# Kernel optimization log

Hardware: AMD Instinct MI355X
Metric: run time of the kernel (lower is better)

## Reference

```python
import jax, jax.numpy as jnp
import numpy as np
import math

D_MODEL = 1024
NUM_HEADS = 16
N_GROUP = 4
HEAD_DIM = D_MODEL // NUM_HEADS  # 64
KV_DIM = N_GROUP * HEAD_DIM      # 256
BS, SEQ = 2, 2048


def setup_inputs() -> dict:
    key = jax.random.key(0)
    ks = jax.random.split(key, 7)
    s = 0.02
    return {
        "h": jax.random.normal(ks[0], (BS, SEQ, D_MODEL), dtype=jnp.float32),
        "wq_w": jax.random.normal(ks[1], (D_MODEL, D_MODEL), dtype=jnp.float32) * s,
        "wq_b": jnp.zeros((D_MODEL,), dtype=jnp.float32),
        "wk_w": jax.random.normal(ks[2], (KV_DIM, D_MODEL), dtype=jnp.float32) * s,
        "wk_b": jnp.zeros((KV_DIM,), dtype=jnp.float32),
        "wv_w": jax.random.normal(ks[3], (KV_DIM, D_MODEL), dtype=jnp.float32) * s,
        "wv_b": jnp.zeros((KV_DIM,), dtype=jnp.float32),
    }


def reference(h, wq_w, wq_b, wk_w, wk_b, wv_w, wv_b):
    bs, seq, _ = h.shape
    rep = NUM_HEADS // N_GROUP  # heads per KV group

    # Linear projections (torch Linear: x @ W.T + b)
    q = h @ wq_w.T + wq_b                     # [bs, seq, d_model]
    k = h @ wk_w.T + wk_b                     # [bs, seq, kv_dim]
    v = h @ wv_w.T + wv_b                     # [bs, seq, kv_dim]

    q = q.reshape(bs, seq, NUM_HEADS, HEAD_DIM).transpose(0, 2, 1, 3)  # [b,H,s,d]
    k = k.reshape(bs, seq, N_GROUP, HEAD_DIM)                          # [b,s,G,d]
    v = v.reshape(bs, seq, N_GROUP, HEAD_DIM)
    # torch .repeat(1,1,1,rep).view(...,num_heads,head_dim) maps head h -> group h//rep,
    # identical to repeating each group `rep` times consecutively along the head axis.
    k = jnp.repeat(k, rep, axis=2).transpose(0, 2, 1, 3)               # [b,H,s,d]
    v = jnp.repeat(v, rep, axis=2).transpose(0, 2, 1, 3)               # [b,H,s,d]

    scores = jnp.einsum("bhqd,bhkd->bhqk", q, k) / math.sqrt(HEAD_DIM)
    attn = jax.nn.softmax(scores, axis=-1)
    out = jnp.einsum("bhqk,bhkd->bhqd", attn, v)                       # [b,H,s,d]
    out = out.transpose(0, 2, 1, 3).reshape(bs, seq, NUM_HEADS * HEAD_DIM)
    return out
```

## Files before the change

### kernel.cpp

```cpp
#include <hip/hip_runtime.h>

typedef _Float16 f16;
typedef _Float16 f16x8 __attribute__((ext_vector_type(8)));
typedef _Float16 f16x4 __attribute__((ext_vector_type(4)));
typedef float f32x4 __attribute__((ext_vector_type(4)));

#define MFMA16(a, b, c) __builtin_amdgcn_mfma_f32_16x16x32_f16((a), (b), (c), 0, 0, 0)

#define SEQ 2048
#define DMODEL 1024
#define NH 16
#define NG 4
#define PAD 76

__device__ __forceinline__ f16x8 cvt8(const float4 a, const float4 b) {
    f16x8 r;
    r[0] = (f16)a.x; r[1] = (f16)a.y; r[2] = (f16)a.z; r[3] = (f16)a.w;
    r[4] = (f16)b.x; r[5] = (f16)b.y; r[6] = (f16)b.z; r[7] = (f16)b.w;
    return r;
}

__device__ __forceinline__ void gl_lds16(f16* lds, const f16* g) {
    __builtin_amdgcn_global_load_lds(
        (const __attribute__((address_space(1))) void*)g,
        (__attribute__((address_space(3))) void*)lds, 16, 0, 0);
}

#define HN  (4096 * 1024)
#define WQN (1024 * 1024)
#define WKN (256 * 1024)
#define WVN (256 * 1024)
#define TOT8 ((HN + WQN + WKN + WVN) / 8)

__global__ __launch_bounds__(256) void cvt_kernel(const float* __restrict__ h,
                                                  const float* __restrict__ wq,
                                                  const float* __restrict__ wk,
                                                  const float* __restrict__ wv,
                                                  f16* __restrict__ h16,
                                                  f16* __restrict__ W16) {
    const int c = blockIdx.x * 256 + threadIdx.x;
    if (c >= TOT8) return;
    const size_t e = (size_t)c * 8;
    const float* src;
    f16* dst;
    if (e < HN) {
        src = h + e; dst = h16 + e;
    } else {
        const size_t e2 = e - HN;
        if (e2 < WQN)            src = wq + e2;
        else if (e2 < WQN + WKN) src = wk + (e2 - WQN);
        else                     src = wv + (e2 - WQN - WKN);
        dst = W16 + e2;
    }
    const float4 a = *(const float4*)src;
    const float4 b = *(const float4*)(src + 4);
    *(f16x8*)dst = cvt8(a, b);
}

__global__ __launch_bounds__(256, 3) void qkv_gemm16(const f16* __restrict__ A,
                                                     const f16* __restrict__ W,
                                                     const float* __restrict__ bq,
                                                     const float* __restrict__ bk,
                                                     const float* __restrict__ bv,
                                                     f16* __restrict__ Qb,
                                                     f16* __restrict__ Kb,
                                                     f16* __restrict__ Vtb,
                                                     float qscale) {
    __shared__ __align__(16) f16 As[2][64 * 32];
    __shared__ __align__(16) f16 Bs[2][128 * 32];

    const int tid  = threadIdx.x;
    const int lane = tid & 63;
    const int l15  = lane & 15;
    const int l4   = lane >> 4;
    const int wave = tid >> 6;
    const int wm   = (wave >> 1) * 32;
    const int wn   = (wave & 1) * 64;
    const int bx   = blockIdx.x;
    const int m0   = blockIdx.y * 64;
    const int n0g  = bx * 128;

    const f16* Ag = A + ((size_t)(m0 + (lane >> 2))) * 1024 + (lane & 3) * 8;
    const f16* Wg = W + ((size_t)(n0g + (lane >> 2))) * 1024 + (lane & 3) * 8;
    const size_t rstep = (size_t)16 * 1024;

    f32x4 acc[2][4];
#pragma unroll
    for (int i = 0; i < 2; i++)
#pragma unroll
        for (int j = 0; j < 4; j++) acc[i][j] = (f32x4)0.0f;

    gl_lds16(&As[0][wave * 512],        Ag + (size_t)wave * rstep);
    gl_lds16(&Bs[0][wave * 1024],       Wg + (size_t)(wave * 2) * rstep);
    gl_lds16(&Bs[0][wave * 1024 + 512], Wg + (size_t)(wave * 2 + 1) * rstep);

    int cur = 0;
    for (int k0 = 0; k0 < DMODEL; k0 += 32) {
        __syncthreads();
        if (k0 + 32 < DMODEL) {
            const int nxt = cur ^ 1;
            const int kn = k0 + 32;
            gl_lds16(&As[nxt][wave * 512],        Ag + (size_t)wave * rstep + kn);
            gl_lds16(&Bs[nxt][wave * 1024],       Wg + (size_t)(wave * 2) * rstep + kn);
            gl_lds16(&Bs[nxt][wave * 1024 + 512], Wg + (size_t)(wave * 2 + 1) * rstep + kn);
        }

        const f16* Ab = As[cur];
        const f16* Bb = Bs[cur];
        f16x8 af[2], bf[4];
#pragma unroll
        for (int i = 0; i < 2; i++)
            af[i] = *(const f16x8*)&Ab[(wm + i * 16 + l15) * 32 + l4 * 8];
#pragma unroll
        for (int j = 0; j < 4; j++)
            bf[j] = *(const f16x8*)&Bb[(wn + j * 16 + l15) * 32 + l4 * 8];
        __builtin_amdgcn_s_setprio(1);
#pragma unroll
        for (int i = 0; i < 2; i++)
#pragma unroll
            for (int j = 0; j < 4; j++)
                acc[i][j] = MFMA16(af[i], bf[j], acc[i][j]);
        __builtin_amdgcn_s_setprio(0);
        cur ^= 1;
    }

    const float* bias; f16* C; int N, n0; float osc; int vmode;
    if (bx < 8)       { bias = bq; C = Qb;  N = 1024; n0 = bx * 128;        osc = qscale; vmode = 0; }
    else if (bx < 10) { bias = bk; C = Kb;  N = 256;  n0 = (bx - 8) * 128;  osc = 1.0f;   vmode = 0; }
    else              { bias = bv; C = Vtb; N = 256;  n0 = (bx - 10) * 128; osc = 1.0f;   vmode = 1; }

#pragma unroll
    for (int i = 0; i < 2; i++) {
        const int mbase = m0 + wm + i * 16 + l4 * 4;
#pragma unroll
        for (int j = 0; j < 4; j++) {
            const int n  = n0 + wn + j * 16 + l15;
            const float bb = bias[n];
            if (vmode == 0) {
#pragma unroll
                for (int r = 0; r < 4; r++)
                    C[(size_t)(mbase + r) * N + n] = (f16)((acc[i][j][r] + bb) * osc);
            } else {
                f16x4 p;
#pragma unroll
                for (int r = 0; r < 4; r++)
                    p[r] = (f16)((acc[i][j][r] + bb) * osc);
                const int batch = mbase >> 11;
                const int s     = mbase & 2047;
                *(f16x4*)&C[((size_t)(batch * 256 + n)) * SEQ + s] = p;
            }
        }
    }
}

__global__ __launch_bounds__(256, 2) void attn_kernel(const f16* __restrict__ Q,
                                                      const f16* __restrict__ Kt,
                                                      const f16* __restrict__ Vt,
                                                      float* __restrict__ out) {
    __shared__ __align__(16) f16 Ks[2][64 * PAD];
    __shared__ __align__(16) f16 Vs[2][64 * PAD];
    __shared__ __align__(16) f16 Ps[128 * PAD];

    const int tid  = threadIdx.x;
    const int lane = tid & 63;
    const int l15  = lane & 15;
    const int l4   = lane >> 4;
    const int wave = tid >> 6;
    const int b    = blockIdx.z;
    const int hh   = blockIdx.y;
    const int g    = hh >> 2;
    const int q0   = blockIdx.x * 128;
    const int qw   = wave * 32;

    f16x8 qf[2][2];
#pragma unroll
    for (int rg = 0; rg < 2; rg++)
#pragma unroll
        for (int kt = 0; kt < 2; kt++)
            qf[rg][kt] = *(const f16x8*)&Q[((size_t)(b * SEQ + q0 + qw + rg * 16 + l15)) * DMODEL
                                           + hh * 64 + kt * 32 + l4 * 8];

    f32x4 oacc[2][4];
    float lsum[2] = {0.0f, 0.0f};
#pragma unroll
    for (int rg = 0; rg < 2; rg++)
#pragma unroll
        for (int dt = 0; dt < 4; dt++) oacc[rg][dt] = (f32x4)0.0f;

    const int srow = tid >> 2;
    const int sc8  = (tid & 3) * 8;
    const f16* Kg = Kt + (size_t)(b * SEQ + srow) * 256 + g * 64 + sc8;
    const f16* Vg = Vt + (size_t)(b * 256 + g * 64 + srow) * SEQ + sc8;

    {
        const f16x8 k0 = *(const f16x8*)(Kg);
        const f16x8 k1 = *(const f16x8*)(Kg + 32);
        const f16x8 v0 = *(const f16x8*)(Vg);
        const f16x8 v1 = *(const f16x8*)(Vg + 32);
        *(f16x8*)&Ks[0][srow * PAD + sc8]      = k0;
        *(f16x8*)&Ks[0][srow * PAD + 32 + sc8] = k1;
        *(f16x8*)&Vs[0][srow * PAD + sc8]      = v0;
        *(f16x8*)&Vs[0][srow * PAD + 32 + sc8] = v1;
    }
    __syncthreads();

    int cur = 0;
    for (int kb = 0; kb < SEQ; kb += 64) {
        const bool more = (kb + 64) < SEQ;
        f16x8 rk0, rk1, rv0, rv1;
        if (more) {
            rk0 = *(const f16x8*)(Kg + (size_t)(kb + 64) * 256);
            rk1 = *(const f16x8*)(Kg + (size_t)(kb + 64) * 256 + 32);
            rv0 = *(const f16x8*)(Vg + kb + 64);
            rv1 = *(const f16x8*)(Vg + kb + 64 + 32);
        }

        f32x4 sacc[2][4];
#pragma unroll
        for (int rg = 0; rg < 2; rg++)
#pragma unroll
            for (int jt = 0; jt < 4; jt++) sacc[rg][jt] = (f32x4)0.0f;
#pragma unroll
        for (int jt = 0; jt < 4; jt++) {
            const f16x8 kf0 = *(const f16x8*)&Ks[cur][(jt * 16 + l15) * PAD + l4 * 8];
            const f16x8 kf1 = *(const f16x8*)&Ks[cur][(jt * 16 + l15) * PAD + 32 + l4 * 8];
#pragma unroll
            for (int rg = 0; rg < 2; rg++) {
                sacc[rg][jt] = MFMA16(kf0, qf[rg][0], sacc[rg][jt]);
                sacc[rg][jt] = MFMA16(kf1, qf[rg][1], sacc[rg][jt]);
            }
        }

#pragma unroll
        for (int rg = 0; rg < 2; rg++)
#pragma unroll
            for (int jt = 0; jt < 4; jt++) {
                f16x4 pp;
#pragma unroll
                for (int r = 0; r < 4; r++) {
                    const float p = exp2f(fminf(sacc[rg][jt][r], 14.0f));
                    lsum[rg] += p;
                    pp[r] = (f16)p;
                }
                *(f16x4*)&Ps[(qw + rg * 16 + l15) * PAD + jt * 16 + l4 * 4] = pp;
            }

#pragma unroll
        for (int kt = 0; kt < 2; kt++) {
            const f16x8 pf0 = *(const f16x8*)&Ps[(qw + l15) * PAD + kt * 32 + l4 * 8];
            const f16x8 pf1 = *(const f16x8*)&Ps[(qw + 16 + l15) * PAD + kt * 32 + l4 * 8];
#pragma unroll
            for (int dt = 0; dt < 4; dt++) {
                const f16x8 vf = *(const f16x8*)&Vs[cur][(dt * 16 + l15) * PAD + kt * 32 + l4 * 8];
                oacc[0][dt] = MFMA16(pf0, vf, oacc[0][dt]);
                oacc[1][dt] = MFMA16(pf1, vf, oacc[1][dt]);
            }
        }

        if (more) {
            const int nxt = cur ^ 1;
            *(f16x8*)&Ks[nxt][srow * PAD + sc8]      = rk0;
            *(f16x8*)&Ks[nxt][srow * PAD + 32 + sc8] = rk1;
            *(f16x8*)&Vs[nxt][srow * PAD + sc8]      = rv0;
            *(f16x8*)&Vs[nxt][srow * PAD + 32 + sc8] = rv1;
        }
        __syncthreads();
        cur ^= 1;
    }

#pragma unroll
    for (int rg = 0; rg < 2; rg++) {
        lsum[rg] += __shfl_xor(lsum[rg], 16);
        lsum[rg] += __shfl_xor(lsum[rg], 32);
    }

#pragma unroll
    for (int rg = 0; rg < 2; rg++)
#pragma unroll
        for (int r = 0; r < 4; r++) {
            const float lv  = __shfl(lsum[rg], l4 * 4 + r);
            const float inv = 1.0f / lv;
            const int q = q0 + qw + rg * 16 + l4 * 4 + r;
            float* op = out + ((size_t)(b * SEQ + q)) * DMODEL + hh * 64;
#pragma unroll
            for (int dt = 0; dt < 4; dt++)
                op[dt * 16 + l15] = oacc[rg][dt][r] * inv;
        }
}

extern "C" void kernel_launch(void* const* d_in, const int* in_sizes, int n_in,
                              void* d_out, int out_size, void* d_ws, size_t ws_size,
                              hipStream_t stream) {
    const float* h    = (const float*)d_in[0];
    const float* wq_w = (const float*)d_in[1];
    const float* wq_b = (const float*)d_in[2];
    const float* wk_w = (const float*)d_in[3];
    const float* wk_b = (const float*)d_in[4];
    const float* wv_w = (const float*)d_in[5];
    const float* wv_b = (const float*)d_in[6];
    float* out = (float*)d_out;

    char* ws = (char*)d_ws;
    f16* Qb  = (f16*)(ws + 0);
    f16* Kb  = (f16*)(ws + 8388608);
    f16* Vtb = (f16*)(ws + 10485760);
    f16* h16 = (f16*)(ws + 12582912);
    f16* W16 = (f16*)(ws + 20971520);

    const float qscale = 0.125f * 1.4426950408889634f;

    cvt_kernel<<<dim3(TOT8 / 256), 256, 0, stream>>>(h, wq_w, wk_w, wv_w, h16, W16);
    qkv_gemm16<<<dim3(12, 64), 256, 0, stream>>>(h16, W16, wq_b, wk_b, wv_b,
                                                 Qb, Kb, Vtb, qscale);
    attn_kernel<<<dim3(16, 16, 2), 256, 0, stream>>>(Qb, Kb, Vtb, out);
}
```

Before: 175.2 us.

## Software-pipeline PV MFMAs one iteration behind QK and softmax

Loads the P and V fragments from LDS into registers at the end of each iteration and issues the P·V MFMAs at the start of the next one, with a final drain after the loop. This interleaves the P·V matrix work with the next tile's QK MFMAs and exp computation, so the matrix units stay busy while softmax runs. In exchange it holds 12 extra f16x8 registers per thread, which raises register pressure and may lower occupancy.

```diff
diff --git a/kernel.cpp b/kernel.cpp
--- a/kernel.cpp
+++ b/kernel.cpp
@@ -204,15 +204,30 @@
     }
     __syncthreads();
 
+    f16x8 pfp[2][2];
+    f16x8 vfp[2][4];
+
     int cur = 0;
-    for (int kb = 0; kb < SEQ; kb += 64) {
-        const bool more = (kb + 64) < SEQ;
+    for (int t = 0; t < 32; t++) {
+        const int kb   = t * 64;
+        const bool more = t < 31;
+
         f16x8 rk0, rk1, rv0, rv1;
         if (more) {
             rk0 = *(const f16x8*)(Kg + (size_t)(kb + 64) * 256);
             rk1 = *(const f16x8*)(Kg + (size_t)(kb + 64) * 256 + 32);
             rv0 = *(const f16x8*)(Vg + kb + 64);
             rv1 = *(const f16x8*)(Vg + kb + 64 + 32);
+        }
+
+        if (t > 0) {
+#pragma unroll
+            for (int kt = 0; kt < 2; kt++)
+#pragma unroll
+                for (int dt = 0; dt < 4; dt++) {
+                    oacc[0][dt] = MFMA16(pfp[kt][0], vfp[kt][dt], oacc[0][dt]);
+                    oacc[1][dt] = MFMA16(pfp[kt][1], vfp[kt][dt], oacc[1][dt]);
+                }
         }
 
         f32x4 sacc[2][4];
@@ -247,14 +262,11 @@
 
 #pragma unroll
         for (int kt = 0; kt < 2; kt++) {
-            const f16x8 pf0 = *(const f16x8*)&Ps[(qw + l15) * PAD + kt * 32 + l4 * 8];
-            const f16x8 pf1 = *(const f16x8*)&Ps[(qw + 16 + l15) * PAD + kt * 32 + l4 * 8];
-#pragma unroll
-            for (int dt = 0; dt < 4; dt++) {
-                const f16x8 vf = *(const f16x8*)&Vs[cur][(dt * 16 + l15) * PAD + kt * 32 + l4 * 8];
-                oacc[0][dt] = MFMA16(pf0, vf, oacc[0][dt]);
-                oacc[1][dt] = MFMA16(pf1, vf, oacc[1][dt]);
-            }
+            pfp[kt][0] = *(const f16x8*)&Ps[(qw + l15) * PAD + kt * 32 + l4 * 8];
+            pfp[kt][1] = *(const f16x8*)&Ps[(qw + 16 + l15) * PAD + kt * 32 + l4 * 8];
+#pragma unroll
+            for (int dt = 0; dt < 4; dt++)
+                vfp[kt][dt] = *(const f16x8*)&Vs[cur][(dt * 16 + l15) * PAD + kt * 32 + l4 * 8];
         }
 
         if (more) {
@@ -267,6 +279,14 @@
         __syncthreads();
         cur ^= 1;
     }
+
+#pragma unroll
+    for (int kt = 0; kt < 2; kt++)
+#pragma unroll
+        for (int dt = 0; dt < 4; dt++) {
+            oacc[0][dt] = MFMA16(pfp[kt][0], vfp[kt][dt], oacc[0][dt]);
+            oacc[1][dt] = MFMA16(pfp[kt][1], vfp[kt][dt], oacc[1][dt]);
+        }
 
 #pragma unroll
     for (int rg = 0; rg < 2; rg++) {
```

After: 173.6 us. No clear change (-0.9%).
